# Kernel optimization log

Measured on AMD Instinct MI355X. Metric: run time of the kernel, lower is better.

The kernel has to match this reference:

```python
import jax, jax.numpy as jnp
import numpy as np

B, S, N = 8, 4, 64
ATOM_FDIM, BOND_FDIM, H = 133, 147, 300
DEPTH = 3


def setup_inputs() -> dict:
    key = jax.random.key(0)
    ks = jax.random.split(key, 9)
    f_atoms = jax.random.normal(ks[0], (B, S, N, ATOM_FDIM), dtype=jnp.float32)
    f_bonds = jax.random.uniform(ks[1], (B, S, N, N, BOND_FDIM), dtype=jnp.float32)
    adj = (jax.random.uniform(ks[2], (B, S, N, N)) < 0.3).astype(jnp.float32)
    def lin(k, fan_in, fan_out):
        return jax.random.normal(k, (fan_in, fan_out), dtype=jnp.float32) / np.sqrt(fan_in)
    return {
        'f_atoms': f_atoms,
        'f_bonds': f_bonds,
        'adj': adj,
        'W_i_atom': lin(ks[3], ATOM_FDIM, H),   # bias=False
        'W_i_bond': lin(ks[4], BOND_FDIM, H),   # bias=False
        'W_h_0': lin(ks[5], H, H),              # bias=False
        'W_h_1': lin(ks[6], H, H),              # bias=False
        'W_o': lin(ks[7], 3 * H, H),            # bias=True
        'b_o': jax.random.normal(ks[8], (H,), dtype=jnp.float32) * 0.01,
    }


def reference(f_atoms, f_bonds, adj, W_i_atom, W_i_bond, W_h_0, W_h_1, W_o, b_o):
    act = jax.nn.relu
    # atom / bond input embeddings
    input_atom = act(f_atoms @ W_i_atom)                        # [B,S,N,H]
    message_atom = input_atom
    input_bond = act((adj[..., None] * f_bonds) @ W_i_bond)     # [B,S,N,N,H]
    message_bond = input_bond
    for W_h in (W_h_0, W_h_1):  # depth-1 message-passing steps
        agg = message_bond.sum(axis=2) * jax.nn.sigmoid(message_bond.max(axis=2))  # [B,S,N,H]
        message_atom = message_atom + agg
        resonance = jnp.einsum('bsnd,bsmd->bsnm', message_atom, message_atom) * adj  # [B,S,N,N]
        # broadcast atom messages along edges, subtract reverse message
        mb = adj[..., None] * message_atom[:, :, None, :, :] - message_bond  # [B,S,N,N,H]
        mb = jnp.swapaxes(mb, 2, 3)  # permute(0,1,3,2,4)
        mb = act(input_bond + mb @ W_h)
        message_bond = mb * jax.nn.softmax(resonance, axis=2)[..., None]
    agg = message_bond.sum(axis=2) * jax.nn.sigmoid(message_bond.max(axis=2))
    a_input = jnp.concatenate([agg, message_atom, input_atom], axis=-1)  # [B,S,N,3H]
    atom_hiddens = act(a_input @ W_o + b_o)  # [B,S,N,H]
    return atom_hiddens, message_bond
```

## Files before the change

### kernel.cpp

```cpp
#include <hip/hip_runtime.h>
#include <hip/hip_bf16.h>
#include <math.h>

#define Bc 8
#define Sc 4
#define Nc 64
#define AF 133
#define BFD 147
#define Hc 300
#define BS (Bc*Sc)
#define ROWS (BS*Nc)
#define EDGES (BS*Nc*Nc)
#define BSLICE 19456
#define BHALF  9728

typedef float f32x4 __attribute__((ext_vector_type(4)));
typedef short bf16x8 __attribute__((ext_vector_type(8)));
typedef float f32x4v __attribute__((ext_vector_type(4)));
typedef f32x4v f32x4u __attribute__((aligned(4)));
union U4 { uint4 u; bf16x8 v; };

__device__ __forceinline__ float reluf(float x){ return fmaxf(x, 0.f); }
__device__ __forceinline__ float b2f(unsigned short u){ union{unsigned int i;float f;}v; v.i = ((unsigned int)u)<<16; return v.f; }
__device__ __forceinline__ unsigned short f2b(float f){ __hip_bfloat16 h = __float2bfloat16(f); return *reinterpret_cast<unsigned short*>(&h); }
__device__ __forceinline__ void split2(float x, unsigned short &hi, unsigned short &lo){
    unsigned short h = f2b(x);
    float r = x - b2f(h);
    hi = h; lo = f2b(r);
}

typedef __attribute__((address_space(1))) const unsigned int* gas1_t;
typedef __attribute__((address_space(3))) unsigned int* las3_t;
__device__ __forceinline__ void gload_lds16(const void* g, void* l){
    __builtin_amdgcn_global_load_lds((gas1_t)g, (las3_t)l, 16, 0, 0);
}

__device__ __forceinline__ void bar_only(){
    __builtin_amdgcn_sched_barrier(0);
    asm volatile("" ::: "memory");
    __builtin_amdgcn_s_barrier();
    asm volatile("" ::: "memory");
    __builtin_amdgcn_sched_barrier(0);
}
__device__ __forceinline__ void bar_drain(){
    __builtin_amdgcn_sched_barrier(0);
    asm volatile("s_waitcnt vmcnt(0) lgkmcnt(0)" ::: "memory");
    __builtin_amdgcn_s_barrier();
    asm volatile("" ::: "memory");
    __builtin_amdgcn_sched_barrier(0);
}

__global__ __launch_bounds__(320) void k_atom_embed(const float* __restrict__ f_atoms,
        const float* __restrict__ W, float* __restrict__ input_atom, float* __restrict__ message_atom){
    __shared__ float x[AF];
    int row = blockIdx.x;
    const float* fr = f_atoms + (size_t)row*AF;
    for (int d = threadIdx.x; d < AF; d += blockDim.x) x[d] = fr[d];
    __syncthreads();
    int h = threadIdx.x;
    if (h < Hc){
        float acc = 0.f;
        for (int d = 0; d < AF; ++d) acc = fmaf(x[d], W[d*Hc + h], acc);
        float v = reluf(acc);
        input_atom[(size_t)row*Hc + h] = v;
        message_atom[(size_t)row*Hc + h] = v;
    }
}

__global__ __launch_bounds__(256) void k_prep_wp2(const float* __restrict__ W, int K, int NKT,
        unsigned short* __restrict__ WP){
    int idx = blockIdx.x*256 + threadIdx.x;
    if (idx >= NKT*BSLICE) return;
    int j  = idx & 7;
    int l  = (idx >> 3) & 63;
    int ct = (idx >> 9) % 19;
    int rem = idx / BHALF;
    int hl = rem & 1;
    int kt = rem >> 1;
    int col = ct*16 + (l & 15);
    int k   = kt*32 + (l >> 4)*8 + j;
    float v = (col < Hc && k < K) ? W[k*Hc + col] : 0.f;
    unsigned short hi, lo; split2(v, hi, lo);
    WP[idx] = hl ? lo : hi;
}

template<int MODE>
__global__ __launch_bounds__(1024) void k_gemm_t(
        const float* __restrict__ Asrc,
        const unsigned short* __restrict__ WP,
        const float* __restrict__ ma,
        const float* __restrict__ adj,
        const float* __restrict__ sm,
        const float* __restrict__ ib,
        float* __restrict__ dst,
        float* __restrict__ aggb)
{
    constexpr int NKT  = (MODE != 0) ? 10 : 5;
    constexpr int ASTR = (MODE != 0) ? 300 : BFD;

    __shared__ unsigned short sAhi[4096];
    __shared__ unsigned short sAlo[4096];
    __shared__ unsigned short sB[BSLICE];
    __shared__ int s_eOut[128];
    __shared__ int s_eRev[128];
    __shared__ float s_adjRev[128];
    __shared__ int s_aAtom[128];

    const int t = threadIdx.x;
    const int bs0 = blockIdx.x >> 5;
    const int mp0 = blockIdx.x & 31;

    if constexpr (MODE == 1){
        if (t < 128){
            int r = t;
            int bs = blockIdx.x >> 5, kk = blockIdx.x & 31;
            int s1 = 64-kk, s2 = 127-2*kk, s3 = 128-kk;
            int a, b;
            if (r < s1){ a = kk; b = kk + r; }
            else if (r < s2){ a = kk+1 + (r - s1); b = kk; }
            else if (r < s3){ a = 63-kk; b = 63-kk + (r - s2); }
            else { a = 64-kk + (r - s3); b = 63-kk; }
            int eo = (bs*64 + a)*64 + b;
            int er = (bs*64 + b)*64 + a;
            s_eOut[r] = eo; s_eRev[r] = er; s_aAtom[r] = bs*64 + a;
            s_adjRev[r] = adj[er];
        }
        __syncthreads();
    }

    const int rt_b = t >> 7;
    const int q_b  = (t >> 5) & 3;
    const int li_b = (t >> 1) & 15;
    const int half = t & 1;
    const int brow = rt_b*16 + li_b;
    const int koff = q_b*8 + 4*half;
    const float* aRow;
    const float* mRow = nullptr;
    float adjR = 0.f;
    if constexpr (MODE == 1){
        aRow = Asrc + (size_t)s_eRev[brow]*ASTR;
        mRow = ma + (size_t)s_aAtom[brow]*Hc;
        adjR = s_adjRev[brow];
    } else if constexpr (MODE == 2){
        int n = brow & 63, cc = brow >> 6;
        int eR = (bs0*64 + (2*mp0 + cc))*64 + n;
        aRow = Asrc + (size_t)eR*ASTR;
        mRow = ma + (size_t)(bs0*64 + n)*Hc;
        adjR = adj[eR];
    } else {
        int n = brow & 63, cc = brow >> 6;
        int e = (bs0*64 + n)*64 + (2*mp0 + cc);
        aRow = Asrc + (size_t)e*ASTR;
        adjR = adj[e];
    }

    float pm[4], pa[4];
    auto prefetchA = [&](int kt){
        int k0 = kt*32 + koff;
        if constexpr (MODE != 0){
            if (k0 <= 296){
                float4 v = *(const float4*)(aRow + k0);
                float4 w = *(const float4*)(mRow + k0);
                pm[0]=v.x; pm[1]=v.y; pm[2]=v.z; pm[3]=v.w;
                pa[0]=w.x; pa[1]=w.y; pa[2]=w.z; pa[3]=w.w;
            }
        } else {
            if (k0 + 3 < BFD){
                f32x4u v = *(const f32x4u*)(aRow + k0);
                pm[0]=v.x; pm[1]=v.y; pm[2]=v.z; pm[3]=v.w;
            } else {
                #pragma unroll
                for (int j = 0; j < 4; ++j){
                    int k = k0 + j;
                    pm[j] = (k < BFD) ? aRow[k] : 0.f;
                }
            }
        }
    };
    auto buildA = [&](int kt){
        int k0 = kt*32 + koff;
        float xv[4];
        if constexpr (MODE != 0){
            if (k0 <= 296){
                #pragma unroll
                for (int j = 0; j < 4; ++j) xv[j] = fmaf(adjR, pa[j], -pm[j]);
            } else { xv[0]=xv[1]=xv[2]=xv[3]=0.f; }
        } else {
            #pragma unroll
            for (int j = 0; j < 4; ++j) xv[j] = adjR * pm[j];
        }
        unsigned short h0,l0,h1,l1,h2,l2,h3,l3;
        split2(xv[0],h0,l0); split2(xv[1],h1,l1);
        split2(xv[2],h2,l2); split2(xv[3],h3,l3);
        uint2 hw, lw;
        hw.x = (unsigned int)h0 | ((unsigned int)h1<<16);
        hw.y = (unsigned int)h2 | ((unsigned int)h3<<16);
        lw.x = (unsigned int)l0 | ((unsigned int)l1<<16);
        lw.y = (unsigned int)l2 | ((unsigned int)l3<<16);
        *(uint2*)&sAhi[4*t] = hw;
        *(uint2*)&sAlo[4*t] = lw;
    };
    auto copyB = [&](int kt){
        const unsigned short* src = WP + (size_t)kt*BSLICE;
        #pragma unroll
        for (int rep = 0; rep < 3; ++rep){
            int i = t + rep*1024;
            if (i < BSLICE/8)
                gload_lds16(src + (size_t)i*8, &sB[i*8]);
        }
    };

    const int wv = t >> 6, lane = t & 63;
    const int li = lane & 15, quad = lane >> 4;
    const int rg = wv & 3;
    const int cg = wv >> 2;
    const int c0 = cg*5;
    const int myC = (cg < 3) ? 5 : 4;

    f32x4 acc[5][2];
    #pragma unroll
    for (int c = 0; c < 5; ++c){ acc[c][0] = (f32x4){0,0,0,0}; acc[c][1] = (f32x4){0,0,0,0}; }

    prefetchA(0);

    if constexpr (MODE != 0){
        #pragma unroll
        for (int c = 0; c < 5; ++c){
            if (c < myC){
                int h = (c0 + c)*16 + li;
                if (h < Hc){
                    #pragma unroll
                    for (int r2 = 0; r2 < 2; ++r2)
                        #pragma unroll
                        for (int i = 0; i < 4; ++i){
                            int row = (2*rg + r2)*16 + quad*4 + i;
                            int e;
                            if constexpr (MODE == 1) e = s_eOut[row];
                            else e = (bs0*64 + (row & 63))*64 + (2*mp0 + (row >> 6));
                            acc[c][r2][i] = ib[(size_t)e*Hc + h];
                        }
                }
            }
        }
    }

    for (int kt = 0; kt < NKT; ++kt){
        if (kt) bar_only();
        copyB(kt);
        buildA(kt);
        bar_drain();
        if (kt+1 < NKT) prefetchA(kt+1);
        __builtin_amdgcn_s_setprio(1);
        U4 a0h, a0l, a1h, a1l;
        a0h.u = *(const uint4*)&sAhi[((2*rg  )*64 + lane)*8];
        a0l.u = *(const uint4*)&sAlo[((2*rg  )*64 + lane)*8];
        a1h.u = *(const uint4*)&sAhi[((2*rg+1)*64 + lane)*8];
        a1l.u = *(const uint4*)&sAlo[((2*rg+1)*64 + lane)*8];
        #pragma unroll
        for (int c = 0; c < 5; ++c){
            if (c < myC){
                U4 bh, bl;
                bh.u = *(const uint4*)&sB[        (c0+c)*512 + lane*8];
                bl.u = *(const uint4*)&sB[BHALF + (c0+c)*512 + lane*8];
                acc[c][0] = __builtin_amdgcn_mfma_f32_16x16x32_bf16(a0h.v, bl.v, acc[c][0], 0,0,0);
                acc[c][0] = __builtin_amdgcn_mfma_f32_16x16x32_bf16(a0l.v, bh.v, acc[c][0], 0,0,0);
                acc[c][0] = __builtin_amdgcn_mfma_f32_16x16x32_bf16(a0h.v, bh.v, acc[c][0], 0,0,0);
                acc[c][1] = __builtin_amdgcn_mfma_f32_16x16x32_bf16(a1h.v, bl.v, acc[c][1], 0,0,0);
                acc[c][1] = __builtin_amdgcn_mfma_f32_16x16x32_bf16(a1l.v, bh.v, acc[c][1], 0,0,0);
                acc[c][1] = __builtin_amdgcn_mfma_f32_16x16x32_bf16(a1h.v, bh.v, acc[c][1], 0,0,0);
            }
        }
        __builtin_amdgcn_s_setprio(0);
    }

    if constexpr (MODE == 1){
        int eO[2][4]; float smv[2][4];
        #pragma unroll
        for (int r2 = 0; r2 < 2; ++r2)
            #pragma unroll
            for (int i = 0; i < 4; ++i){
                int row = (2*rg + r2)*16 + quad*4 + i;
                int e = s_eOut[row];
                eO[r2][i] = e;
                smv[r2][i] = sm[e];
            }
        #pragma unroll
        for (int c = 0; c < 5; ++c){
            if (c >= myC) continue;
            int h = (c0 + c)*16 + li;
            if (h >= Hc) continue;
            #pragma unroll
            for (int r2 = 0; r2 < 2; ++r2)
                #pragma unroll
                for (int i = 0; i < 4; ++i){
                    size_t off = (size_t)eO[r2][i]*Hc + h;
                    dst[off] = reluf(acc[c][r2][i]) * smv[r2][i];
                }
        }
    } else {
        __syncthreads();
        float* sRedS = (float*)sB;
        float* sRedM = sRedS + 16*304;
        int eO[2][4]; float smv[2][4];
        #pragma unroll
        for (int r2 = 0; r2 < 2; ++r2)
            #pragma unroll
            for (int i = 0; i < 4; ++i){
                int row = (2*rg + r2)*16 + quad*4 + i;
                int e = (bs0*64 + (row & 63))*64 + (2*mp0 + (row >> 6));
                eO[r2][i] = e;
                if constexpr (MODE == 2) smv[r2][i] = sm[e];
            }
        #pragma unroll
        for (int c = 0; c < 5; ++c){
            float s8 = 0.f, m8 = -INFINITY;
            int h = (c0 + c)*16 + li;
            if (c < myC && h < Hc){
                #pragma unroll
                for (int r2 = 0; r2 < 2; ++r2)
                    #pragma unroll
                    for (int i = 0; i < 4; ++i){
                        float v = reluf(acc[c][r2][i]);
                        if constexpr (MODE == 2) v *= smv[r2][i];
                        dst[(size_t)eO[r2][i]*Hc + h] = v;
                        s8 += v; m8 = fmaxf(m8, v);
                    }
            }
            s8 += __shfl_xor(s8, 16, 64); s8 += __shfl_xor(s8, 32, 64);
            m8 = fmaxf(m8, __shfl_xor(m8, 16, 64)); m8 = fmaxf(m8, __shfl_xor(m8, 32, 64));
            if (c < myC && quad == 0){
                sRedS[wv*304 + (c0 + c)*16 + li] = s8;
                sRedM[wv*304 + (c0 + c)*16 + li] = m8;
            }
        }
        __syncthreads();
        if (t < 608){
            int cc = t / 304, h = t - cc*304;
            if (h < Hc){
                int ct = h >> 4;
                int cgf = (ct < 15) ? (ct/5) : 3;
                int w0 = (cgf << 2) + 2*cc;
                float s = sRedS[w0*304 + h] + sRedS[(w0+1)*304 + h];
                float m = fmaxf(sRedM[w0*304 + h], sRedM[(w0+1)*304 + h]);
                float agg = s * (1.f/(1.f + expf(-m)));
                size_t o = (size_t)(bs0*64 + 2*mp0 + cc)*Hc + h;
                if constexpr (MODE == 0) aggb[o] += agg;
                else                     aggb[o]  = agg;
            }
        }
    }
}

__global__ __launch_bounds__(256) void k_ma_add(float* __restrict__ ma, const float* __restrict__ aggb){
    int i = blockIdx.x*256 + threadIdx.x;
    if (i < ROWS*Hc/4){
        float4 a = ((const float4*)aggb)[i];
        float4 v = ((float4*)ma)[i];
        v.x += a.x; v.y += a.y; v.z += a.z; v.w += a.w;
        ((float4*)ma)[i] = v;
    }
}

__global__ __launch_bounds__(320) void k_agg(const float* __restrict__ message_bond,
        float* __restrict__ message_atom, float* __restrict__ agg_out, int final_mode){
    int t = threadIdx.x;
    int r = t / 80, c = t - r*80;
    if (c >= 75) return;
    int row = blockIdx.x*4 + r;
    int bs = row >> 6, m = row & 63;
    size_t base = ((size_t)(bs*Nc)*Nc + m)*(size_t)Hc + (size_t)c*4;
    float4 s  = {0.f, 0.f, 0.f, 0.f};
    float4 mx = {-INFINITY, -INFINITY, -INFINITY, -INFINITY};
    #pragma unroll 4
    for (int n = 0; n < Nc; ++n){
        float4 v = *(const float4*)(message_bond + base + (size_t)n*Nc*Hc);
        s.x += v.x; s.y += v.y; s.z += v.z; s.w += v.w;
        mx.x = fmaxf(mx.x, v.x); mx.y = fmaxf(mx.y, v.y);
        mx.z = fmaxf(mx.z, v.z); mx.w = fmaxf(mx.w, v.w);
    }
    float4 agg;
    agg.x = s.x * (1.f/(1.f + expf(-mx.x)));
    agg.y = s.y * (1.f/(1.f + expf(-mx.y)));
    agg.z = s.z * (1.f/(1.f + expf(-mx.z)));
    agg.w = s.w * (1.f/(1.f + expf(-mx.w)));
    size_t o = (size_t)row*Hc + (size_t)c*4;
    if (final_mode){
        *(float4*)(agg_out + o) = agg;
    } else {
        float4 cur = *(const float4*)(message_atom + o);
        cur.x += agg.x; cur.y += agg.y; cur.z += agg.z; cur.w += agg.w;
        *(float4*)(message_atom + o) = cur;
    }
}

__global__ __launch_bounds__(256) void k_resonance_softmax(const float* __restrict__ message_atom,
        const float* __restrict__ adj, float* __restrict__ sm){
    int bs = blockIdx.x >> 6, m = blockIdx.x & 63;
    __shared__ float am[Hc];
    __shared__ float res[Nc];
    for (int d = threadIdx.x; d < Hc; d += blockDim.x)
        am[d] = message_atom[((size_t)(bs*Nc)+m)*Hc + d];
    __syncthreads();
    int wave = threadIdx.x >> 6, lane = threadIdx.x & 63;
    for (int n = wave; n < Nc; n += 4){
        const float* man = message_atom + ((size_t)(bs*Nc)+n)*Hc;
        float acc = 0.f;
        for (int d = lane; d < Hc; d += 64) acc = fmaf(man[d], am[d], acc);
        #pragma unroll
        for (int off = 32; off > 0; off >>= 1) acc += __shfl_xor(acc, off, 64);
        if (lane == 0) res[n] = acc * adj[((size_t)(bs*Nc)+n)*Nc + m];
    }
    __syncthreads();
    if (threadIdx.x < Nc){
        float v = res[threadIdx.x];
        float mx = v;
        #pragma unroll
        for (int off = 32; off > 0; off >>= 1) mx = fmaxf(mx, __shfl_xor(mx, off, 64));
        float e = expf(v - mx);
        float ssum = e;
        #pragma unroll
        for (int off = 32; off > 0; off >>= 1) ssum += __shfl_xor(ssum, off, 64);
        sm[((size_t)(bs*Nc)+threadIdx.x)*Nc + m] = e / ssum;
    }
}

#define R7 4
__global__ __launch_bounds__(320) void k_output(const float* __restrict__ agg,
        const float* __restrict__ message_atom, const float* __restrict__ input_atom,
        const float* __restrict__ W_o, const float* __restrict__ b_o, float* __restrict__ out){
    __shared__ float xin[R7][3*Hc];
    int r0 = blockIdx.x * R7;
    for (int idx = threadIdx.x; idx < R7*3*Hc; idx += blockDim.x){
        int r = idx / (3*Hc), k = idx - r*(3*Hc);
        int row = r0 + r;
        float v;
        if (k < Hc)           v = agg[(size_t)row*Hc + k];
        else if (k < 2*Hc)    v = message_atom[(size_t)row*Hc + (k - Hc)];
        else                  v = input_atom[(size_t)row*Hc + (k - 2*Hc)];
        xin[r][k] = v;
    }
    __syncthreads();
    int h = threadIdx.x;
    if (h < Hc){
        float acc[R7];
        #pragma unroll
        for (int r=0;r<R7;r++) acc[r] = b_o[h];
        for (int d = 0; d < 3*Hc; ++d){
            float w = W_o[d*Hc + h];
            #pragma unroll
            for (int r=0;r<R7;r++) acc[r] = fmaf(xin[r][d], w, acc[r]);
        }
        #pragma unroll
        for (int r=0;r<R7;r++) out[(size_t)(r0+r)*Hc + h] = reluf(acc[r]);
    }
}

extern "C" void kernel_launch(void* const* d_in, const int* in_sizes, int n_in,
                              void* d_out, int out_size, void* d_ws, size_t ws_size,
                              hipStream_t stream){
    const float* f_atoms  = (const float*)d_in[0];
    const float* f_bonds  = (const float*)d_in[1];
    const float* adj      = (const float*)d_in[2];
    const float* W_i_atom = (const float*)d_in[3];
    const float* W_i_bond = (const float*)d_in[4];
    const float* W_h0     = (const float*)d_in[5];
    const float* W_h1     = (const float*)d_in[6];
    const float* W_o      = (const float*)d_in[7];
    const float* b_o      = (const float*)d_in[8];

    float* out = (float*)d_out;
    float* atom_hiddens = out;
    float* mb_out = out + (size_t)ROWS*Hc;

    float* wsf = (float*)d_ws;
    float* input_atom   = wsf; wsf += (size_t)ROWS*Hc;
    float* message_atom = wsf; wsf += (size_t)ROWS*Hc;
    float* sm           = wsf; wsf += (size_t)EDGES;
    float* aggb         = wsf; wsf += (size_t)ROWS*Hc;
    float* ib           = wsf; wsf += (size_t)EDGES*Hc;
    unsigned short* wsu = (unsigned short*)wsf;
    unsigned short* WP0 = wsu; wsu += 10*BSLICE;
    unsigned short* WP1 = wsu; wsu += 10*BSLICE;
    unsigned short* WPb = wsu; wsu += 5*BSLICE;
    float* agg_out = ib;

    k_atom_embed<<<ROWS, 320, 0, stream>>>(f_atoms, W_i_atom, input_atom, message_atom);
    k_prep_wp2<<<(10*BSLICE + 255)/256, 256, 0, stream>>>(W_h0, Hc, 10, WP0);
    k_prep_wp2<<<(10*BSLICE + 255)/256, 256, 0, stream>>>(W_h1, Hc, 10, WP1);
    k_prep_wp2<<<(5*BSLICE + 255)/256, 256, 0, stream>>>(W_i_bond, BFD, 5, WPb);
    k_gemm_t<0><<<BS*32, 1024, 0, stream>>>(f_bonds, WPb, nullptr, adj, nullptr, nullptr, ib, message_atom);
    k_resonance_softmax<<<ROWS, 256, 0, stream>>>(message_atom, adj, sm);
    k_gemm_t<2><<<BS*32, 1024, 0, stream>>>(ib, WP0, message_atom, adj, sm, ib, mb_out, aggb);
    k_ma_add<<<(ROWS*Hc/4 + 255)/256, 256, 0, stream>>>(message_atom, aggb);
    k_resonance_softmax<<<ROWS, 256, 0, stream>>>(message_atom, adj, sm);
    k_gemm_t<1><<<BS*32, 1024, 0, stream>>>(mb_out, WP1, message_atom, adj, sm, ib, mb_out, nullptr);
    k_agg<<<ROWS/4, 320, 0, stream>>>(mb_out, nullptr, agg_out, 1);
    k_output<<<ROWS/R7, 320, 0, stream>>>(agg_out, message_atom, input_atom, W_o, b_o, atom_hiddens);
}
```

Baseline: 754.1 us.

## Fuse second-layer aggregation into GEMM via extra workspace buffer; widen A staging

When workspace allows, the first message-passing GEMM writes to a separate buffer. The second layer can then use MODE 2, which fuses the sum/max/sigmoid aggregation into the GEMM epilogue, and the separate k_agg launch is dropped. A-tile staging now loads 8 floats per thread for a pair of K-tiles, with alternating waves building each tile. The ib preload and the output stores are reordered to go row by row, and launch bounds gain a min-blocks hint. This costs one extra edge-sized buffer and may raise register pressure.

```diff
diff --git a/kernel.cpp b/kernel.cpp
--- a/kernel.cpp
+++ b/kernel.cpp
@@ -85,7 +85,7 @@
 }
 
 template<int MODE>
-__global__ __launch_bounds__(1024) void k_gemm_t(
+__global__ __launch_bounds__(1024, 8) void k_gemm_t(
         const float* __restrict__ Asrc,
         const unsigned short* __restrict__ WP,
         const float* __restrict__ ma,
@@ -97,6 +97,7 @@
 {
     constexpr int NKT  = (MODE != 0) ? 10 : 5;
     constexpr int ASTR = (MODE != 0) ? 300 : BFD;
+    constexpr int KLIM = (MODE != 0) ? 300 : BFD;
 
     __shared__ unsigned short sAhi[4096];
     __shared__ unsigned short sAlo[4096];
@@ -113,7 +114,7 @@
     if constexpr (MODE == 1){
         if (t < 128){
             int r = t;
-            int bs = blockIdx.x >> 5, kk = blockIdx.x & 31;
+            int bs = bs0, kk = mp0;
             int s1 = 64-kk, s2 = 127-2*kk, s3 = 128-kk;
             int a, b;
             if (r < s1){ a = kk; b = kk + r; }
@@ -128,12 +129,13 @@
         __syncthreads();
     }
 
-    const int rt_b = t >> 7;
-    const int q_b  = (t >> 5) & 3;
-    const int li_b = (t >> 1) & 15;
-    const int half = t & 1;
-    const int brow = rt_b*16 + li_b;
-    const int koff = q_b*8 + 4*half;
+    const int rt_b  = t >> 7;
+    const int li_b  = (t >> 1) & 15;
+    const int brow  = rt_b*16 + li_b;
+    const int j0    = ((t>>5)&3)*16 + (t&1)*8;
+    const int wvpar = (t>>6)&1;
+    const int ks0   = j0 & 31;
+
     const float* aRow;
     const float* mRow = nullptr;
     float adjR = 0.f;
@@ -154,51 +156,66 @@
         adjR = adj[e];
     }
 
-    float pm[4], pa[4];
-    auto prefetchA = [&](int kt){
-        int k0 = kt*32 + koff;
+    float pm[8], pa[8];
+    auto prefetchPair = [&](int kp){
+        int k0 = kp*64 + j0;
         if constexpr (MODE != 0){
-            if (k0 <= 296){
-                float4 v = *(const float4*)(aRow + k0);
-                float4 w = *(const float4*)(mRow + k0);
-                pm[0]=v.x; pm[1]=v.y; pm[2]=v.z; pm[3]=v.w;
-                pa[0]=w.x; pa[1]=w.y; pa[2]=w.z; pa[3]=w.w;
-            }
-        } else {
-            if (k0 + 3 < BFD){
-                f32x4u v = *(const f32x4u*)(aRow + k0);
-                pm[0]=v.x; pm[1]=v.y; pm[2]=v.z; pm[3]=v.w;
+            if (k0 + 7 < KLIM){
+                float4 v0 = *(const float4*)(aRow + k0);
+                float4 v1 = *(const float4*)(aRow + k0 + 4);
+                float4 w0 = *(const float4*)(mRow + k0);
+                float4 w1 = *(const float4*)(mRow + k0 + 4);
+                pm[0]=v0.x; pm[1]=v0.y; pm[2]=v0.z; pm[3]=v0.w;
+                pm[4]=v1.x; pm[5]=v1.y; pm[6]=v1.z; pm[7]=v1.w;
+                pa[0]=w0.x; pa[1]=w0.y; pa[2]=w0.z; pa[3]=w0.w;
+                pa[4]=w1.x; pa[5]=w1.y; pa[6]=w1.z; pa[7]=w1.w;
             } else {
                 #pragma unroll
-                for (int j = 0; j < 4; ++j){
-                    int k = k0 + j;
-                    pm[j] = (k < BFD) ? aRow[k] : 0.f;
+                for (int jj = 0; jj < 8; ++jj){
+                    int k = k0 + jj; bool ok = (k < KLIM);
+                    pm[jj] = ok ? aRow[k] : 0.f;
+                    pa[jj] = ok ? mRow[k] : 0.f;
                 }
             }
+        } else {
+            if (k0 + 7 < KLIM){
+                f32x4u v0 = *(const f32x4u*)(aRow + k0);
+                f32x4u v1 = *(const f32x4u*)(aRow + k0 + 4);
+                pm[0]=v0.x; pm[1]=v0.y; pm[2]=v0.z; pm[3]=v0.w;
+                pm[4]=v1.x; pm[5]=v1.y; pm[6]=v1.z; pm[7]=v1.w;
+            } else {
+                #pragma unroll
+                for (int jj = 0; jj < 8; ++jj){
+                    int k = k0 + jj;
+                    pm[jj] = (k < KLIM) ? aRow[k] : 0.f;
+                }
+            }
         }
     };
-    auto buildA = [&](int kt){
-        int k0 = kt*32 + koff;
-        float xv[4];
+    auto buildA8 = [&](){
+        float xv[8];
         if constexpr (MODE != 0){
-            if (k0 <= 296){
-                #pragma unroll
-                for (int j = 0; j < 4; ++j) xv[j] = fmaf(adjR, pa[j], -pm[j]);
-            } else { xv[0]=xv[1]=xv[2]=xv[3]=0.f; }
+            #pragma unroll
+            for (int jj = 0; jj < 8; ++jj) xv[jj] = fmaf(adjR, pa[jj], -pm[jj]);
         } else {
             #pragma unroll
-            for (int j = 0; j < 4; ++j) xv[j] = adjR * pm[j];
-        }
-        unsigned short h0,l0,h1,l1,h2,l2,h3,l3;
-        split2(xv[0],h0,l0); split2(xv[1],h1,l1);
-        split2(xv[2],h2,l2); split2(xv[3],h3,l3);
-        uint2 hw, lw;
-        hw.x = (unsigned int)h0 | ((unsigned int)h1<<16);
-        hw.y = (unsigned int)h2 | ((unsigned int)h3<<16);
-        lw.x = (unsigned int)l0 | ((unsigned int)l1<<16);
-        lw.y = (unsigned int)l2 | ((unsigned int)l3<<16);
-        *(uint2*)&sAhi[4*t] = hw;
-        *(uint2*)&sAlo[4*t] = lw;
+            for (int jj = 0; jj < 8; ++jj) xv[jj] = adjR * pm[jj];
+        }
+        unsigned short hh[8], ll[8];
+        #pragma unroll
+        for (int jj = 0; jj < 8; ++jj) split2(xv[jj], hh[jj], ll[jj]);
+        uint4 hw, lw;
+        hw.x = (unsigned)hh[0] | ((unsigned)hh[1]<<16);
+        hw.y = (unsigned)hh[2] | ((unsigned)hh[3]<<16);
+        hw.z = (unsigned)hh[4] | ((unsigned)hh[5]<<16);
+        hw.w = (unsigned)hh[6] | ((unsigned)hh[7]<<16);
+        lw.x = (unsigned)ll[0] | ((unsigned)ll[1]<<16);
+        lw.y = (unsigned)ll[2] | ((unsigned)ll[3]<<16);
+        lw.z = (unsigned)ll[4] | ((unsigned)ll[5]<<16);
+        lw.w = (unsigned)ll[6] | ((unsigned)ll[7]<<16);
+        int idx = rt_b*512 + ((ks0>>3)*16 + li_b)*8;
+        *(uint4*)&sAhi[idx] = hw;
+        *(uint4*)&sAlo[idx] = lw;
     };
     auto copyB = [&](int kt){
         const unsigned short* src = WP + (size_t)kt*BSLICE;
@@ -221,35 +238,36 @@
     #pragma unroll
     for (int c = 0; c < 5; ++c){ acc[c][0] = (f32x4){0,0,0,0}; acc[c][1] = (f32x4){0,0,0,0}; }
 
-    prefetchA(0);
+    prefetchPair(0);
 
     if constexpr (MODE != 0){
         #pragma unroll
-        for (int c = 0; c < 5; ++c){
-            if (c < myC){
-                int h = (c0 + c)*16 + li;
-                if (h < Hc){
-                    #pragma unroll
-                    for (int r2 = 0; r2 < 2; ++r2)
-                        #pragma unroll
-                        for (int i = 0; i < 4; ++i){
-                            int row = (2*rg + r2)*16 + quad*4 + i;
-                            int e;
-                            if constexpr (MODE == 1) e = s_eOut[row];
-                            else e = (bs0*64 + (row & 63))*64 + (2*mp0 + (row >> 6));
-                            acc[c][r2][i] = ib[(size_t)e*Hc + h];
-                        }
+        for (int r2 = 0; r2 < 2; ++r2)
+            #pragma unroll
+            for (int i = 0; i < 4; ++i){
+                int row = (2*rg + r2)*16 + quad*4 + i;
+                int e;
+                if constexpr (MODE == 1) e = s_eOut[row];
+                else e = (bs0*64 + (row & 63))*64 + (2*mp0 + (row >> 6));
+                const float* ibr = ib + (size_t)e*Hc;
+                #pragma unroll
+                for (int c = 0; c < 5; ++c){
+                    if (c < myC){
+                        int h = (c0 + c)*16 + li;
+                        if (h < Hc) acc[c][r2][i] = ibr[h];
+                    }
                 }
             }
-        }
-    }
-
+    }
+
+    #pragma unroll
     for (int kt = 0; kt < NKT; ++kt){
         if (kt) bar_only();
         copyB(kt);
-        buildA(kt);
+        bool bld = ((kt & 1) == wvpar);
+        if (bld) buildA8();
         bar_drain();
-        if (kt+1 < NKT) prefetchA(kt+1);
+        if (bld && (kt + 2 < NKT)) prefetchPair((kt>>1) + 1);
         __builtin_amdgcn_s_setprio(1);
         U4 a0h, a0l, a1h, a1l;
         a0h.u = *(const uint4*)&sAhi[((2*rg  )*64 + lane)*8];
@@ -274,63 +292,59 @@
     }
 
     if constexpr (MODE == 1){
-        int eO[2][4]; float smv[2][4];
         #pragma unroll
         for (int r2 = 0; r2 < 2; ++r2)
             #pragma unroll
             for (int i = 0; i < 4; ++i){
                 int row = (2*rg + r2)*16 + quad*4 + i;
                 int e = s_eOut[row];
-                eO[r2][i] = e;
-                smv[r2][i] = sm[e];
-            }
-        #pragma unroll
-        for (int c = 0; c < 5; ++c){
-            if (c >= myC) continue;
-            int h = (c0 + c)*16 + li;
-            if (h >= Hc) continue;
-            #pragma unroll
-            for (int r2 = 0; r2 < 2; ++r2)
+                float smr = sm[e];
+                float* drow = dst + (size_t)e*Hc;
                 #pragma unroll
-                for (int i = 0; i < 4; ++i){
-                    size_t off = (size_t)eO[r2][i]*Hc + h;
-                    dst[off] = reluf(acc[c][r2][i]) * smv[r2][i];
+                for (int c = 0; c < 5; ++c){
+                    if (c < myC){
+                        int h = (c0 + c)*16 + li;
+                        if (h < Hc) drow[h] = reluf(acc[c][r2][i]) * smr;
+                    }
                 }
-        }
+            }
     } else {
         __syncthreads();
         float* sRedS = (float*)sB;
         float* sRedM = sRedS + 16*304;
-        int eO[2][4]; float smv[2][4];
+        float s8[5], m8[5];
+        #pragma unroll
+        for (int c = 0; c < 5; ++c){ s8[c] = 0.f; m8[c] = -INFINITY; }
         #pragma unroll
         for (int r2 = 0; r2 < 2; ++r2)
             #pragma unroll
             for (int i = 0; i < 4; ++i){
                 int row = (2*rg + r2)*16 + quad*4 + i;
                 int e = (bs0*64 + (row & 63))*64 + (2*mp0 + (row >> 6));
-                eO[r2][i] = e;
-                if constexpr (MODE == 2) smv[r2][i] = sm[e];
+                float smr = 0.f;
+                if constexpr (MODE == 2) smr = sm[e];
+                float* drow = dst + (size_t)e*Hc;
+                #pragma unroll
+                for (int c = 0; c < 5; ++c){
+                    if (c < myC){
+                        int h = (c0 + c)*16 + li;
+                        if (h < Hc){
+                            float v = reluf(acc[c][r2][i]);
+                            if constexpr (MODE == 2) v *= smr;
+                            drow[h] = v;
+                            s8[c] += v; m8[c] = fmaxf(m8[c], v);
+                        }
+                    }
+                }
             }
         #pragma unroll
         for (int c = 0; c < 5; ++c){
-            float s8 = 0.f, m8 = -INFINITY;
-            int h = (c0 + c)*16 + li;
-            if (c < myC && h < Hc){
-                #pragma unroll
-                for (int r2 = 0; r2 < 2; ++r2)
-                    #pragma unroll
-                    for (int i = 0; i < 4; ++i){
-                        float v = reluf(acc[c][r2][i]);
-                        if constexpr (MODE == 2) v *= smv[r2][i];
-                        dst[(size_t)eO[r2][i]*Hc + h] = v;
-                        s8 += v; m8 = fmaxf(m8, v);
-                    }
-            }
-            s8 += __shfl_xor(s8, 16, 64); s8 += __shfl_xor(s8, 32, 64);
-            m8 = fmaxf(m8, __shfl_xor(m8, 16, 64)); m8 = fmaxf(m8, __shfl_xor(m8, 32, 64));
+            float s = s8[c], m = m8[c];
+            s += __shfl_xor(s, 16, 64); s += __shfl_xor(s, 32, 64);
+            m = fmaxf(m, __shfl_xor(m, 16, 64)); m = fmaxf(m, __shfl_xor(m, 32, 64));
             if (c < myC && quad == 0){
-                sRedS[wv*304 + (c0 + c)*16 + li] = s8;
-                sRedM[wv*304 + (c0 + c)*16 + li] = m8;
+                sRedS[wv*304 + (c0 + c)*16 + li] = s;
+                sRedM[wv*304 + (c0 + c)*16 + li] = m;
             }
         }
         __syncthreads();
@@ -482,7 +496,12 @@
     unsigned short* WP0 = wsu; wsu += 10*BSLICE;
     unsigned short* WP1 = wsu; wsu += 10*BSLICE;
     unsigned short* WPb = wsu; wsu += 5*BSLICE;
-    float* agg_out = ib;
+
+    size_t used = (size_t)((char*)wsu - (char*)d_ws);
+    used = (used + 255) & ~(size_t)255;
+    float* mbx = nullptr;
+    if (ws_size >= used + (size_t)EDGES*Hc*sizeof(float))
+        mbx = (float*)((char*)d_ws + used);
 
     k_atom_embed<<<ROWS, 320, 0, stream>>>(f_atoms, W_i_atom, input_atom, message_atom);
     k_prep_wp2<<<(10*BSLICE + 255)/256, 256, 0, stream>>>(W_h0, Hc, 10, WP0);
@@ -490,10 +509,19 @@
     k_prep_wp2<<<(5*BSLICE + 255)/256, 256, 0, stream>>>(W_i_bond, BFD, 5, WPb);
     k_gemm_t<0><<<BS*32, 1024, 0, stream>>>(f_bonds, WPb, nullptr, adj, nullptr, nullptr, ib, message_atom);
     k_resonance_softmax<<<ROWS, 256, 0, stream>>>(message_atom, adj, sm);
-    k_gemm_t<2><<<BS*32, 1024, 0, stream>>>(ib, WP0, message_atom, adj, sm, ib, mb_out, aggb);
-    k_ma_add<<<(ROWS*Hc/4 + 255)/256, 256, 0, stream>>>(message_atom, aggb);
-    k_resonance_softmax<<<ROWS, 256, 0, stream>>>(message_atom, adj, sm);
-    k_gemm_t<1><<<BS*32, 1024, 0, stream>>>(mb_out, WP1, message_atom, adj, sm, ib, mb_out, nullptr);
-    k_agg<<<ROWS/4, 320, 0, stream>>>(mb_out, nullptr, agg_out, 1);
-    k_output<<<ROWS/R7, 320, 0, stream>>>(agg_out, message_atom, input_atom, W_o, b_o, atom_hiddens);
-}
+    if (mbx){
+        k_gemm_t<2><<<BS*32, 1024, 0, stream>>>(ib, WP0, message_atom, adj, sm, ib, mbx, aggb);
+        k_ma_add<<<(ROWS*Hc/4 + 255)/256, 256, 0, stream>>>(message_atom, aggb);
+        k_resonance_softmax<<<ROWS, 256, 0, stream>>>(message_atom, adj, sm);
+        k_gemm_t<2><<<BS*32, 1024, 0, stream>>>(mbx, WP1, message_atom, adj, sm, ib, mb_out, aggb);
+        k_output<<<ROWS/R7, 320, 0, stream>>>(aggb, message_atom, input_atom, W_o, b_o, atom_hiddens);
+    } else {
+        float* agg_out = ib;
+        k_gemm_t<2><<<BS*32, 1024, 0, stream>>>(ib, WP0, message_atom, adj, sm, ib, mb_out, aggb);
+        k_ma_add<<<(ROWS*Hc/4 + 255)/256, 256, 0, stream>>>(message_atom, aggb);
+        k_resonance_softmax<<<ROWS, 256, 0, stream>>>(message_atom, adj, sm);
+        k_gemm_t<1><<<BS*32, 1024, 0, stream>>>(mb_out, WP1, message_atom, adj, sm, ib, mb_out, nullptr);
+        k_agg<<<ROWS/4, 320, 0, stream>>>(mb_out, nullptr, agg_out, 1);
+        k_output<<<ROWS/R7, 320, 0, stream>>>(agg_out, message_atom, input_atom, W_o, b_o, atom_hiddens);
+    }
+}
```

Result: slower. 1.669 ms (+121.3%).
